# Optimization experiments

Hardware: AMD Instinct MI355X
Metric: run time of the kernel (lower is better)

## Reference

```python
import jax, jax.numpy as jnp
import numpy as np

PATCH = 3
ALPHA = 0.1


def _unfold3x3(x):
    # x: [B, C, H, W] -> [B, C*9, H, W], torch F.unfold with k=3, pad=1, stride=1
    B, C, H, W = x.shape
    p = PATCH // 2
    xp = jnp.pad(x, ((0, 0), (0, 0), (p, p), (p, p)))
    shifts = [xp[:, :, i:i + H, j:j + W] for i in range(PATCH) for j in range(PATCH)]
    # torch unfold orders (C, kh, kw); ordering is irrelevant for the dot-product
    # correlation, but we match it anyway: stack kernel positions after channel.
    out = jnp.stack(shifts, axis=2)  # [B, C, 9, H, W]
    return out.reshape(B, C * PATCH * PATCH, H, W)


def setup_inputs() -> dict:
    key = jax.random.key(0)
    k1, k2 = jax.random.split(key)
    x_lab = jax.random.normal(k1, (4, 3, 64, 64), dtype=jnp.float32)
    feature = jax.random.normal(k2, (4, 64, 64, 64), dtype=jnp.float32)
    return {"x_lab": x_lab, "feature": feature}


def reference(x_lab, feature):
    # scale_factor=1 and feature already at (H, W): both interpolates are identity.
    B, _, H, W = x_lab.shape
    N = H * W
    x_ab = x_lab.reshape(B, 3, N).transpose(0, 2, 1)          # [B, N, 3]
    lf = _unfold3x3(feature).reshape(B, -1, N)                 # [B, C*9, N]
    corr = jnp.einsum('bcn,bcm->bnm', lf, lf)                  # [B, N, N]
    attn = jax.nn.softmax(corr / ALPHA, axis=-1)
    weighted = jnp.einsum('bnm,bmc->bnc', attn, x_ab)          # [B, N, 3]
    return weighted.transpose(0, 2, 1).reshape(B, 3, H, W)
```

## Files before the change

### kernel.cpp

```cpp
#include <hip/hip_runtime.h>


#define NPIX 4096
#define ROWCH 528
#define ROWB  (ROWCH * 16)
#define SCALE 10.0f

typedef __attribute__((ext_vector_type(8))) short bf16x8;
typedef __attribute__((ext_vector_type(4))) float f32x4;

#define MF(a, b, c) __builtin_amdgcn_mfma_f32_16x16x32_bf16(a, b, c, 0, 0, 0)

__device__ __forceinline__ uint4 pack8(const float* v) {
    unsigned h[8];
#pragma unroll
    for (int j = 0; j < 8; ++j) {
        unsigned u = __float_as_uint(v[j]);
        u = u + 0x7fffu + ((u >> 16) & 1u);
        h[j] = u >> 16;
    }
    return (uint4){h[0] | (h[1] << 16), h[2] | (h[3] << 16),
                   h[4] | (h[5] << 16), h[6] | (h[7] << 16)};
}

__device__ __forceinline__ void load_row(const float* fr, int kc, int x, float* L) {
#pragma unroll
    for (int j = 0; j < 8; ++j) L[j] = fr[(size_t)(kc * 8 + j) * NPIX + x];
}

#define MFMA_GRP(T, DBASE) do {                                               \
    _Pragma("unroll")                                                         \
    for (int dx = 0; dx < 3; ++dx)                                            \
        _Pragma("unroll")                                                     \
        for (int ks = 0; ks < 2; ++ks) {                                      \
            acc[T][0] = MF(AF[((DBASE) + dx) * 2 + ks], Bf[ks][0][dx], acc[T][0]); \
            acc[T][1] = MF(AF[((DBASE) + dx) * 2 + ks], Bf[ks][1][dx], acc[T][1]); \
        }                                                                     \
} while (0)

#define RETIRE(S, myv) do {                                                   \
    _Pragma("unroll")                                                         \
    for (int kt = 0; kt < 2; ++kt) {                                          \
        const int kx = kh * 32 + kt * 16 + nl;                                \
        const float xv0 = xls[(myv) * 64 + kx];                               \
        const float xv1 = xls[NPIX + (myv) * 64 + kx];                        \
        const float xv2 = xls[2 * NPIX + (myv) * 64 + kx];                    \
        _Pragma("unroll")                                                     \
        for (int rg = 0; rg < 4; ++rg) {                                      \
            const float e = __expf(fmaf(acc[S][kt][rg], SCALE, negM[rg]));    \
            l_[rg] += e;                                                      \
            A0[rg] = fmaf(e, xv0, A0[rg]);                                    \
            A1[rg] = fmaf(e, xv1, A1[rg]);                                    \
            A2[rg] = fmaf(e, xv2, A2[rg]);                                    \
        }                                                                     \
        acc[S][kt] = (f32x4){0.f, 0.f, 0.f, 0.f};                             \
    }                                                                         \
} while (0)

#define STEP(RM, SN, SR, rr) do {                                             \
    const int r_ = (rr);                                                      \
    if (r_ <= 61) *(uint4*)(ring + (SR) * ROWB + wu16) = pack8(L);            \
    if (r_ <= 60) load_row(featb + (r_ + 3) * 64, kc, x, L);                  \
    if (r_ < 64) {                                                            \
        const char* base = ring + (RM) * ROWB + bu;                           \
        bf16x8 Bf[2][2][3];                                                   \
        _Pragma("unroll")                                                     \
        for (int ks = 0; ks < 2; ++ks)                                        \
            _Pragma("unroll")                                                 \
            for (int kt = 0; kt < 2; ++kt) {                                  \
                const char* p = base + (ks * 264 + kt * 16) * 16;             \
                Bf[ks][kt][0] = *(const bf16x8*)(p);                          \
                Bf[ks][kt][1] = *(const bf16x8*)(p + 16);                     \
                Bf[ks][kt][2] = *(const bf16x8*)(p + 32);                     \
            }                                                                 \
        if (r_ >= 1)     MFMA_GRP(SR, 6);           \
        MFMA_GRP(RM, 3);                                    \
        if (r_ + 1 < 64) MFMA_GRP(SN, 0);                   \
    }                                                                         \
    if (r_ >= 1 && r_ <= 64) RETIRE(SR, r_ - 1);                              \
    if (r_ < 64) __syncthreads();                                             \
} while (0)

__global__ __launch_bounds__(512)
__attribute__((amdgpu_waves_per_eu(2, 2)))
void nlwa_fused(const float* __restrict__ x_lab,
                const float* __restrict__ feature,
                float* __restrict__ out)
{
    __shared__ __align__(16) char ring[3 * ROWB];
    __shared__ float xls[3 * NPIX];
    __shared__ float part[3][8][64];
    __shared__ float ssq[3][64];
    __shared__ float4 scrF[64][2];

    const int tid = threadIdx.x;
    const int b = blockIdx.x >> 6, ny = blockIdx.x & 63;
    const int w = tid >> 6, lane = tid & 63;
    const int quad = lane >> 4, nl = lane & 15;
    const int qw = w & 3, kh = w >> 2;
    const int kc = w, x = lane;
    const int wu16 = (kc * 66 + x + 1) * 16;
    const int bu = (quad * 66 + kh * 32 + nl) * 16;

    const float* featb = feature + (size_t)b * 64 * NPIX;
    const float* xb = x_lab + (size_t)b * 3 * NPIX;

    {
        const float4* s4 = (const float4*)xb;
        float4* d4 = (float4*)xls;
        for (int i = tid; i < 3 * NPIX / 4; i += 512) d4[i] = s4[i];
    }
    if (tid < 48) {
        const int sl = tid / 16, pu = tid % 16;
        const int u = (pu >> 1) * 66 + (pu & 1) * 65;
        *(uint4*)(ring + sl * ROWB + u * 16) = (uint4){0u, 0u, 0u, 0u};
    }

    float L[8];
#pragma unroll
    for (int dyi = 0; dyi < 3; ++dyi) {
        const int qr = ny + dyi - 1;
        float ss = 0.f;
        if (qr >= 0 && qr < 64) {
            load_row(featb + qr * 64, kc, x, L);
#pragma unroll
            for (int j = 0; j < 8; ++j) ss = fmaf(L[j], L[j], ss);
            *(uint4*)(ring + dyi * ROWB + wu16) = pack8(L);
        } else {
            *(uint4*)(ring + dyi * ROWB + wu16) = (uint4){0u, 0u, 0u, 0u};
        }
        part[dyi][kc][x] = ss;
    }
    __syncthreads();

    if (tid < 192) {
        const int dyi = tid >> 6, xx = tid & 63;
        float s = 0.f;
#pragma unroll
        for (int k = 0; k < 8; ++k) s += part[dyi][k][xx];
        ssq[dyi][xx] = s;
    }

    bf16x8 AF[18];
#pragma unroll
    for (int dyi = 0; dyi < 3; ++dyi)
#pragma unroll
        for (int dx = 0; dx < 3; ++dx)
#pragma unroll
            for (int ks = 0; ks < 2; ++ks)
                AF[(dyi * 3 + dx) * 2 + ks] = *(const bf16x8*)(ring + dyi * ROWB +
                    ((quad + ks * 4) * 66 + qw * 16 + nl + dx) * 16);
    __syncthreads();

    float negM[4];
#pragma unroll
    for (int rg = 0; rg < 4; ++rg) {
        const int q = qw * 16 + quad * 4 + rg;
        float a = 0.f;
#pragma unroll
        for (int dyi = 0; dyi < 3; ++dyi)
#pragma unroll
            for (int dx = -1; dx <= 1; ++dx) {
                const int cx = q + dx;
                a += (cx >= 0 && cx < 64) ? ssq[dyi][cx] : 0.f;
            }
        negM[rg] = -SCALE * a;
    }

#pragma unroll
    for (int rr = 0; rr < 2; ++rr) {
        load_row(featb + rr * 64, kc, x, L);
        *(uint4*)(ring + rr * ROWB + wu16) = pack8(L);
    }
    load_row(featb + 2 * 64, kc, x, L);

    float l_[4], A0[4], A1[4], A2[4];
#pragma unroll
    for (int rg = 0; rg < 4; ++rg) { l_[rg] = 0.f; A0[rg] = 0.f; A1[rg] = 0.f; A2[rg] = 0.f; }
    f32x4 acc[3][2];
#pragma unroll
    for (int i = 0; i < 3; ++i) {
        acc[i][0] = (f32x4){0.f, 0.f, 0.f, 0.f};
        acc[i][1] = (f32x4){0.f, 0.f, 0.f, 0.f};
    }
    __syncthreads();

    for (int rb = 0; rb < 66; rb += 3) {
        STEP(0, 1, 2, rb);
        STEP(1, 2, 0, rb + 1);
        STEP(2, 0, 1, rb + 2);
    }

#pragma unroll
    for (int rg = 0; rg < 4; ++rg) {
#pragma unroll
        for (int off = 8; off >= 1; off >>= 1) {
            l_[rg] += __shfl_down(l_[rg], off, 16);
            A0[rg] += __shfl_down(A0[rg], off, 16);
            A1[rg] += __shfl_down(A1[rg], off, 16);
            A2[rg] += __shfl_down(A2[rg], off, 16);
        }
    }
    if (nl == 0) {
#pragma unroll
        for (int rg = 0; rg < 4; ++rg) {
            const int q = qw * 16 + quad * 4 + rg;
            scrF[q][kh] = make_float4(l_[rg], A0[rg], A1[rg], A2[rg]);
        }
    }
    __syncthreads();
    if (tid < 64) {
        const float4 t0 = scrF[tid][0], t1 = scrF[tid][1];
        const float inv = 1.0f / (t0.x + t1.x);
        float* o = out + (size_t)b * 3 * NPIX + ny * 64 + tid;
        o[0]        = (t0.y + t1.y) * inv;
        o[NPIX]     = (t0.z + t1.z) * inv;
        o[2 * NPIX] = (t0.w + t1.w) * inv;
    }
}

extern "C" void kernel_launch(void* const* d_in, const int* in_sizes, int n_in,
                              void* d_out, int out_size, void* d_ws, size_t ws_size,
                              hipStream_t stream) {
    (void)in_sizes; (void)n_in; (void)out_size; (void)d_ws; (void)ws_size;
    const float* x_lab   = (const float*)d_in[0];
    const float* feature = (const float*)d_in[1];
    float* out = (float*)d_out;
    nlwa_fused<<<dim3(256), dim3(512), 0, stream>>>(x_lab, feature, out);
}
```

Measured before the change: 134.4 us.

## Split each query row across two blocks and narrow per-wave key tiles

Launches 512 blocks instead of 256, with each block handling half of a query row (32 queries), and redistributes waves as 2 query groups × 4 key quarters. Each wave now keeps a single accumulator tile instead of two, which halves the MFMA, B-fragment and exp work per wave and frees registers. Launch bounds change from a fixed two waves per EU to a minimum-blocks hint. The intent is to fill all compute units on the MI355X (256 CUs) and raise occupancy. The cost is that every block still streams and bf16-packs the whole key feature map, so global reads and conversion work per output double.

```diff
diff --git a/kernel.cpp b/kernel.cpp
--- a/kernel.cpp
+++ b/kernel.cpp
@@ -32,29 +32,24 @@
     _Pragma("unroll")                                                         \
     for (int dx = 0; dx < 3; ++dx)                                            \
         _Pragma("unroll")                                                     \
-        for (int ks = 0; ks < 2; ++ks) {                                      \
-            acc[T][0] = MF(AF[((DBASE) + dx) * 2 + ks], Bf[ks][0][dx], acc[T][0]); \
-            acc[T][1] = MF(AF[((DBASE) + dx) * 2 + ks], Bf[ks][1][dx], acc[T][1]); \
-        }                                                                     \
+        for (int ks = 0; ks < 2; ++ks)                                        \
+            acc[T] = MF(AF[((DBASE) + dx) * 2 + ks], Bf[ks][dx], acc[T]);     \
 } while (0)
 
 #define RETIRE(S, myv) do {                                                   \
+    const int kx = kq * 16 + nl;                                              \
+    const float xv0 = xls[(myv) * 64 + kx];                                   \
+    const float xv1 = xls[NPIX + (myv) * 64 + kx];                            \
+    const float xv2 = xls[2 * NPIX + (myv) * 64 + kx];                        \
     _Pragma("unroll")                                                         \
-    for (int kt = 0; kt < 2; ++kt) {                                          \
-        const int kx = kh * 32 + kt * 16 + nl;                                \
-        const float xv0 = xls[(myv) * 64 + kx];                               \
-        const float xv1 = xls[NPIX + (myv) * 64 + kx];                        \
-        const float xv2 = xls[2 * NPIX + (myv) * 64 + kx];                    \
-        _Pragma("unroll")                                                     \
-        for (int rg = 0; rg < 4; ++rg) {                                      \
-            const float e = __expf(fmaf(acc[S][kt][rg], SCALE, negM[rg]));    \
-            l_[rg] += e;                                                      \
-            A0[rg] = fmaf(e, xv0, A0[rg]);                                    \
-            A1[rg] = fmaf(e, xv1, A1[rg]);                                    \
-            A2[rg] = fmaf(e, xv2, A2[rg]);                                    \
-        }                                                                     \
-        acc[S][kt] = (f32x4){0.f, 0.f, 0.f, 0.f};                             \
+    for (int rg = 0; rg < 4; ++rg) {                                          \
+        const float e = __expf(fmaf(acc[S][rg], SCALE, negM[rg]));            \
+        l_[rg] += e;                                                          \
+        A0[rg] = fmaf(e, xv0, A0[rg]);                                        \
+        A1[rg] = fmaf(e, xv1, A1[rg]);                                        \
+        A2[rg] = fmaf(e, xv2, A2[rg]);                                        \
     }                                                                         \
+    acc[S] = (f32x4){0.f, 0.f, 0.f, 0.f};                                     \
 } while (0)
 
 #define STEP(RM, SN, SR, rr) do {                                             \
@@ -63,16 +58,14 @@
     if (r_ <= 60) load_row(featb + (r_ + 3) * 64, kc, x, L);                  \
     if (r_ < 64) {                                                            \
         const char* base = ring + (RM) * ROWB + bu;                           \
-        bf16x8 Bf[2][2][3];                                                   \
+        bf16x8 Bf[2][3];                                                      \
         _Pragma("unroll")                                                     \
-        for (int ks = 0; ks < 2; ++ks)                                        \
-            _Pragma("unroll")                                                 \
-            for (int kt = 0; kt < 2; ++kt) {                                  \
-                const char* p = base + (ks * 264 + kt * 16) * 16;             \
-                Bf[ks][kt][0] = *(const bf16x8*)(p);                          \
-                Bf[ks][kt][1] = *(const bf16x8*)(p + 16);                     \
-                Bf[ks][kt][2] = *(const bf16x8*)(p + 32);                     \
-            }                                                                 \
+        for (int ks = 0; ks < 2; ++ks) {                                      \
+            const char* p = base + ks * 4224;                                 \
+            Bf[ks][0] = *(const bf16x8*)(p);                                  \
+            Bf[ks][1] = *(const bf16x8*)(p + 16);                             \
+            Bf[ks][2] = *(const bf16x8*)(p + 32);                             \
+        }                                                                     \
         if (r_ >= 1)     MFMA_GRP(SR, 6);           \
         MFMA_GRP(RM, 3);                                    \
         if (r_ + 1 < 64) MFMA_GRP(SN, 0);                   \
@@ -81,29 +74,29 @@
     if (r_ < 64) __syncthreads();                                             \
 } while (0)
 
-__global__ __launch_bounds__(512)
-__attribute__((amdgpu_waves_per_eu(2, 2)))
+__global__ __launch_bounds__(512, 4)
 void nlwa_fused(const float* __restrict__ x_lab,
                 const float* __restrict__ feature,
                 float* __restrict__ out)
 {
     __shared__ __align__(16) char ring[3 * ROWB];
     __shared__ float xls[3 * NPIX];
-    __shared__ float part[3][8][64];
+    __shared__ __align__(16) char aux[6144];
     __shared__ float ssq[3][64];
-    __shared__ float4 scrF[64][2];
-
     const int tid = threadIdx.x;
-    const int b = blockIdx.x >> 6, ny = blockIdx.x & 63;
+    const int bid = blockIdx.x;
+    const int b = bid >> 7, ny = (bid >> 1) & 63, qh = bid & 1;
     const int w = tid >> 6, lane = tid & 63;
     const int quad = lane >> 4, nl = lane & 15;
-    const int qw = w & 3, kh = w >> 2;
+    const int qg = w & 1, kq = w >> 1;
+    const int qofs = qh * 32 + qg * 16;
     const int kc = w, x = lane;
     const int wu16 = (kc * 66 + x + 1) * 16;
-    const int bu = (quad * 66 + kh * 32 + nl) * 16;
+    const int bu = (quad * 66 + kq * 16 + nl) * 16;
 
     const float* featb = feature + (size_t)b * 64 * NPIX;
     const float* xb = x_lab + (size_t)b * 3 * NPIX;
+    float* part = (float*)aux;
 
     {
         const float4* s4 = (const float4*)xb;
@@ -129,7 +122,7 @@
         } else {
             *(uint4*)(ring + dyi * ROWB + wu16) = (uint4){0u, 0u, 0u, 0u};
         }
-        part[dyi][kc][x] = ss;
+        part[(dyi * 8 + kc) * 64 + x] = ss;
     }
     __syncthreads();
 
@@ -137,7 +130,7 @@
         const int dyi = tid >> 6, xx = tid & 63;
         float s = 0.f;
 #pragma unroll
-        for (int k = 0; k < 8; ++k) s += part[dyi][k][xx];
+        for (int k = 0; k < 8; ++k) s += part[(dyi * 8 + k) * 64 + xx];
         ssq[dyi][xx] = s;
     }
 
@@ -149,13 +142,13 @@
 #pragma unroll
             for (int ks = 0; ks < 2; ++ks)
                 AF[(dyi * 3 + dx) * 2 + ks] = *(const bf16x8*)(ring + dyi * ROWB +
-                    ((quad + ks * 4) * 66 + qw * 16 + nl + dx) * 16);
+                    ((quad + ks * 4) * 66 + qofs + nl + dx) * 16);
     __syncthreads();
 
     float negM[4];
 #pragma unroll
     for (int rg = 0; rg < 4; ++rg) {
-        const int q = qw * 16 + quad * 4 + rg;
+        const int q = qofs + quad * 4 + rg;
         float a = 0.f;
 #pragma unroll
         for (int dyi = 0; dyi < 3; ++dyi)
@@ -177,12 +170,9 @@
     float l_[4], A0[4], A1[4], A2[4];
 #pragma unroll
     for (int rg = 0; rg < 4; ++rg) { l_[rg] = 0.f; A0[rg] = 0.f; A1[rg] = 0.f; A2[rg] = 0.f; }
-    f32x4 acc[3][2];
-#pragma unroll
-    for (int i = 0; i < 3; ++i) {
-        acc[i][0] = (f32x4){0.f, 0.f, 0.f, 0.f};
-        acc[i][1] = (f32x4){0.f, 0.f, 0.f, 0.f};
-    }
+    f32x4 acc[3];
+#pragma unroll
+    for (int i = 0; i < 3; ++i) acc[i] = (f32x4){0.f, 0.f, 0.f, 0.f};
     __syncthreads();
 
     for (int rb = 0; rb < 66; rb += 3) {
@@ -201,21 +191,24 @@
             A2[rg] += __shfl_down(A2[rg], off, 16);
         }
     }
+    __syncthreads();
+    float4* scrF = (float4*)aux;
     if (nl == 0) {
 #pragma unroll
         for (int rg = 0; rg < 4; ++rg) {
-            const int q = qw * 16 + quad * 4 + rg;
-            scrF[q][kh] = make_float4(l_[rg], A0[rg], A1[rg], A2[rg]);
+            const int ql = qg * 16 + quad * 4 + rg;
+            scrF[ql * 4 + kq] = make_float4(l_[rg], A0[rg], A1[rg], A2[rg]);
         }
     }
     __syncthreads();
-    if (tid < 64) {
-        const float4 t0 = scrF[tid][0], t1 = scrF[tid][1];
-        const float inv = 1.0f / (t0.x + t1.x);
-        float* o = out + (size_t)b * 3 * NPIX + ny * 64 + tid;
-        o[0]        = (t0.y + t1.y) * inv;
-        o[NPIX]     = (t0.z + t1.z) * inv;
-        o[2 * NPIX] = (t0.w + t1.w) * inv;
+    if (tid < 32) {
+        const float4 t0 = scrF[tid * 4 + 0], t1 = scrF[tid * 4 + 1];
+        const float4 t2 = scrF[tid * 4 + 2], t3 = scrF[tid * 4 + 3];
+        const float inv = 1.0f / (t0.x + t1.x + t2.x + t3.x);
+        float* o = out + (size_t)b * 3 * NPIX + ny * 64 + qh * 32 + tid;
+        o[0]        = (t0.y + t1.y + t2.y + t3.y) * inv;
+        o[NPIX]     = (t0.z + t1.z + t2.z + t3.z) * inv;
+        o[2 * NPIX] = (t0.w + t1.w + t2.w + t3.w) * inv;
     }
 }
 
@@ -226,5 +219,5 @@
     const float* x_lab   = (const float*)d_in[0];
     const float* feature = (const float*)d_in[1];
     float* out = (float*)d_out;
-    nlwa_fused<<<dim3(256), dim3(512), 0, stream>>>(x_lab, feature, out);
-}
+    nlwa_fused<<<dim3(512), dim3(512), 0, stream>>>(x_lab, feature, out);
+}
```

Result: slower. 329.2 us (+145.0%).
